# Optimization experiments

Hardware: AMD Instinct MI355X
Metric: run time of the kernel (lower is better)

The kernel has to match this reference:

```python
import jax, jax.numpy as jnp
import numpy as np

# Tsit5 Butcher tableau (Tsitouras 2011), 5th-order solution weights.
C2, C3, C4, C5 = 0.161, 0.327, 0.9, 0.9800255409045097
A21 = 0.161
A31, A32 = -0.008480655492356989, 0.335480655492357
A41, A42, A43 = 2.8971530571054935, -6.359448489975075, 4.3622954328695815
A51, A52, A53, A54 = 5.325864828439257, -11.748883564062828, 7.4955393428898365, -0.09249506636175525
A61, A62, A63, A64, A65 = 5.86145544294642, -12.92096931784711, 8.159367898576159, -0.071584973281401, -0.028269050394068383
B1, B2, B3, B4, B5, B6 = 0.09646076681806523, 0.01, 0.4798896504144996, 1.379008574103742, -3.290069515436081, 2.324710524099774


def setup_inputs() -> dict:
    key = jax.random.key(0)
    k0, k1, k2, k3 = jax.random.split(key, 4)
    B, D, W, T = 2048, 64, 128, 50
    y0 = jax.random.normal(k0, (B, D), dtype=jnp.float32)
    ts = (jnp.arange(T, dtype=jnp.float32)) * 0.02  # t0=0, t1=0.98, dt0=0.02
    # equinox-style MLP params (Linear stores weight as [out, in]); scaled for stability
    w0 = jax.random.normal(k1, (W, D + 1), dtype=jnp.float32) / np.sqrt(D + 1)
    b0 = jnp.zeros((W,), dtype=jnp.float32)
    w1 = jax.random.normal(k2, (W, W), dtype=jnp.float32) / np.sqrt(W)
    b1 = jnp.zeros((W,), dtype=jnp.float32)
    w2 = jax.random.normal(k3, (D, W), dtype=jnp.float32) / np.sqrt(W)
    b2 = jnp.zeros((D,), dtype=jnp.float32)
    return {"y0": y0, "ts": ts, "w0": w0, "b0": b0, "w1": w1, "b1": b1, "w2": w2, "b2": b2}


def reference(y0, ts, w0, b0, w1, b1, w2, b2):
    # dynamics f(t, y) = MLP(concat([t, y])), vectorized over batch
    def dyn(t, y):
        tcol = jnp.full((y.shape[0], 1), t, dtype=y.dtype)
        inp = jnp.concatenate([tcol, y], axis=1)           # [B, D+1]
        h = jax.nn.relu(inp @ w0.T + b0)                    # [B, W]
        h = jax.nn.relu(h @ w1.T + b1)                      # [B, W]
        return h @ w2.T + b2                                # [B, D]

    dt = ts[1] - ts[0]

    def step(y, t):
        k1 = dyn(t, y)
        k2 = dyn(t + C2 * dt, y + dt * (A21 * k1))
        k3 = dyn(t + C3 * dt, y + dt * (A31 * k1 + A32 * k2))
        k4 = dyn(t + C4 * dt, y + dt * (A41 * k1 + A42 * k2 + A43 * k3))
        k5 = dyn(t + C5 * dt, y + dt * (A51 * k1 + A52 * k2 + A53 * k3 + A54 * k4))
        k6 = dyn(t + dt, y + dt * (A61 * k1 + A62 * k2 + A63 * k3 + A64 * k4 + A65 * k5))
        y_new = y + dt * (B1 * k1 + B2 * k2 + B3 * k3 + B4 * k4 + B5 * k5 + B6 * k6)
        return y_new, None

    yT, _ = jax.lax.scan(step, y0, ts[:-1])  # 49 constant-size Tsit5 steps
    return yT
```

## Files before the change

### kernel.cpp

```cpp
#include <hip/hip_runtime.h>

typedef __attribute__((ext_vector_type(8))) short short8;
typedef __attribute__((ext_vector_type(4))) float f32x4;
typedef __attribute__((ext_vector_type(4))) unsigned short ushort4v;

__device__ __constant__ float dA2[6][6] = {
  {0.f, 0.f, 0.f, 0.f, 0.f, 0.f},
  {0.161f, 0.f, 0.f, 0.f, 0.f, 0.f},
  {-0.008480655492356989f, 0.335480655492357f, 0.f, 0.f, 0.f, 0.f},
  {2.8971530571054935f, -6.359448489975075f, 4.3622954328695815f, 0.f, 0.f, 0.f},
  {5.325864828439257f, -11.748883564062828f, 7.4955393428898365f, -0.09249506636175525f, 0.f, 0.f},
  {5.86145544294642f, -12.92096931784711f, 8.159367898576159f, -0.071584973281401f, -0.028269050394068383f, 0.f}
};
__device__ __constant__ float dC6[6] = {0.f, 0.161f, 0.327f, 0.9f, 0.9800255409045097f, 1.0f};
__device__ __constant__ float dB6v[6] = {0.09646076681806523f, 0.01f, 0.4798896504144996f,
                                         1.379008574103742f, -3.290069515436081f, 2.324710524099774f};

#define NSTEPS 49
#define XS 136

__device__ __forceinline__ unsigned short f2bf(float f) {
    unsigned u = __builtin_bit_cast(unsigned, f);
    u += 0x7fff + ((u >> 16) & 1);
    return (unsigned short)(u >> 16);
}

extern "C" __global__ void __launch_bounds__(512, 1)
node_solve(const float* __restrict__ y0, const float* __restrict__ ts,
           const float* __restrict__ gw0, const float* __restrict__ gb0,
           const float* __restrict__ gw1, const float* __restrict__ gb1,
           const float* __restrict__ gw2, const float* __restrict__ gb2,
           float* __restrict__ out)
{
    __shared__ __align__(16) unsigned short sSI[16 * XS];
    __shared__ __align__(16) unsigned short sH1[16 * XS];
    __shared__ __align__(16) unsigned short sH2[16 * XS];

    const int tid  = threadIdx.x;
    const int w    = tid >> 6;
    const int lane = tid & 63;
    const int q    = lane >> 4;
    const int c    = lane & 15;
    const int nt   = 16 * w;
    const int n3   = 16 * w;
    const int row0 = blockIdx.x * 16;

    for (int i = tid; i < 16 * 48; i += 512) {
        int r = i / 48, j = i - r * 48;
        ((int*)sSI)[r * 68 + j] = 0;
    }
    __syncthreads();
    for (int i = tid; i < 16 * 64; i += 512) {
        int r = i >> 6, d = i & 63;
        sSI[r * XS + d] = f2bf(y0[(size_t)(row0 + r) * 64 + d]);
    }
    if (tid < 16) sSI[tid * XS + 64] = f2bf(ts[0]);

    short8 wL1[3], wL2[4], wL3[4];
    float  bL1, bL2, bL3 = 0.f;
    {
        const int n = nt + c;
        #pragma unroll
        for (int ks = 0; ks < 3; ++ks) {
            short8 v;
            #pragma unroll
            for (int j = 0; j < 8; ++j) {
                const int k = ks * 32 + q * 8 + j;
                float f = (k < 64) ? gw0[n * 65 + 1 + k] : (k == 64 ? gw0[n * 65] : 0.f);
                v[j] = (short)f2bf(f);
            }
            wL1[ks] = v;
        }
        #pragma unroll
        for (int ks = 0; ks < 4; ++ks) {
            short8 v;
            #pragma unroll
            for (int j = 0; j < 8; ++j) v[j] = (short)f2bf(gw1[n * 128 + ks * 32 + q * 8 + j]);
            wL2[ks] = v;
        }
        bL1 = gb0[n]; bL2 = gb1[n];
    }
    if (w < 4) {
        const int n = n3 + c;
        #pragma unroll
        for (int ks = 0; ks < 4; ++ks) {
            short8 v;
            #pragma unroll
            for (int j = 0; j < 8; ++j) v[j] = (short)f2bf(gw2[n * 128 + ks * 32 + q * 8 + j]);
            wL3[ks] = v;
        }
        bL3 = gb2[n];
    }

    float sy[4] = {0.f, 0.f, 0.f, 0.f};
    float k0[4], k1[4], k2[4], k3[4], k4[4], k5[4];
    #pragma unroll
    for (int r = 0; r < 4; ++r) { k0[r]=0.f; k1[r]=0.f; k2[r]=0.f; k3[r]=0.f; k4[r]=0.f; k5[r]=0.f; }
    if (w < 4) {
        #pragma unroll
        for (int r = 0; r < 4; ++r)
            sy[r] = y0[(size_t)(row0 + c) * 64 + n3 + q * 4 + r];
    }

    const float ts0 = ts[0];
    const float dtv = ts[1] - ts[0];

    __syncthreads();

    #pragma unroll 1
    for (int step = 0; step < NSTEPS; ++step) {
        const float tstep = ts0 + (float)step * dtv;

        #pragma unroll
        for (int s = 0; s < 6; ++s) {
            {
                const unsigned short* xb = &sSI[c * XS + q * 8];
                short8 x0 = *(const short8*)(xb);
                short8 x1 = *(const short8*)(xb + 32);
                short8 x2 = *(const short8*)(xb + 64);
                f32x4 a0 = {0.f,0.f,0.f,0.f};
                a0 = __builtin_amdgcn_mfma_f32_16x16x32_bf16(wL1[0], x0, a0, 0, 0, 0);
                a0 = __builtin_amdgcn_mfma_f32_16x16x32_bf16(wL1[1], x1, a0, 0, 0, 0);
                a0 = __builtin_amdgcn_mfma_f32_16x16x32_bf16(wL1[2], x2, a0, 0, 0, 0);
                ushort4v o0;
                #pragma unroll
                for (int r = 0; r < 4; ++r) o0[r] = f2bf(fmaxf(a0[r] + bL1, 0.f));
                *(ushort4v*)(&sH1[c * XS + nt + q * 4]) = o0;
            }
            __syncthreads();

            {
                const unsigned short* xb = &sH1[c * XS + q * 8];
                short8 x0 = *(const short8*)(xb);
                short8 x1 = *(const short8*)(xb + 32);
                short8 x2 = *(const short8*)(xb + 64);
                short8 x3 = *(const short8*)(xb + 96);
                f32x4 a0 = {0.f,0.f,0.f,0.f}, a1 = {0.f,0.f,0.f,0.f};
                a0 = __builtin_amdgcn_mfma_f32_16x16x32_bf16(wL2[0], x0, a0, 0, 0, 0);
                a1 = __builtin_amdgcn_mfma_f32_16x16x32_bf16(wL2[1], x1, a1, 0, 0, 0);
                a0 = __builtin_amdgcn_mfma_f32_16x16x32_bf16(wL2[2], x2, a0, 0, 0, 0);
                a1 = __builtin_amdgcn_mfma_f32_16x16x32_bf16(wL2[3], x3, a1, 0, 0, 0);
                a0 = a0 + a1;
                ushort4v o0;
                #pragma unroll
                for (int r = 0; r < 4; ++r) o0[r] = f2bf(fmaxf(a0[r] + bL2, 0.f));
                *(ushort4v*)(&sH2[c * XS + nt + q * 4]) = o0;
            }
            __syncthreads();

            if (w < 4) {
                const unsigned short* xb = &sH2[c * XS + q * 8];
                short8 x0 = *(const short8*)(xb);
                short8 x1 = *(const short8*)(xb + 32);
                short8 x2 = *(const short8*)(xb + 64);
                short8 x3 = *(const short8*)(xb + 96);
                f32x4 aa = {0.f,0.f,0.f,0.f}, ab = {0.f,0.f,0.f,0.f};
                aa = __builtin_amdgcn_mfma_f32_16x16x32_bf16(wL3[0], x0, aa, 0, 0, 0);
                ab = __builtin_amdgcn_mfma_f32_16x16x32_bf16(wL3[1], x1, ab, 0, 0, 0);
                aa = __builtin_amdgcn_mfma_f32_16x16x32_bf16(wL3[2], x2, aa, 0, 0, 0);
                ab = __builtin_amdgcn_mfma_f32_16x16x32_bf16(wL3[3], x3, ab, 0, 0, 0);
                aa = aa + ab;

                float kv[4];
                #pragma unroll
                for (int r = 0; r < 4; ++r) kv[r] = aa[r] + bL3;
                if      (s == 0) { k0[0]=kv[0]; k0[1]=kv[1]; k0[2]=kv[2]; k0[3]=kv[3]; }
                else if (s == 1) { k1[0]=kv[0]; k1[1]=kv[1]; k1[2]=kv[2]; k1[3]=kv[3]; }
                else if (s == 2) { k2[0]=kv[0]; k2[1]=kv[1]; k2[2]=kv[2]; k2[3]=kv[3]; }
                else if (s == 3) { k3[0]=kv[0]; k3[1]=kv[1]; k3[2]=kv[2]; k3[3]=kv[3]; }
                else if (s == 4) { k4[0]=kv[0]; k4[1]=kv[1]; k4[2]=kv[2]; k4[3]=kv[3]; }
                else             { k5[0]=kv[0]; k5[1]=kv[1]; k5[2]=kv[2]; k5[3]=kv[3]; }

                float si[4];
                if (s < 5) {
                    const float a0c = dA2[s + 1][0], a1c = dA2[s + 1][1], a2c = dA2[s + 1][2];
                    const float a3c = dA2[s + 1][3], a4c = dA2[s + 1][4], a5c = dA2[s + 1][5];
                    #pragma unroll
                    for (int r = 0; r < 4; ++r)
                        si[r] = sy[r] + dtv * (a0c*k0[r] + a1c*k1[r] + a2c*k2[r]
                                             + a3c*k3[r] + a4c*k4[r] + a5c*k5[r]);
                } else {
                    #pragma unroll
                    for (int r = 0; r < 4; ++r) {
                        sy[r] += dtv * (dB6v[0]*k0[r] + dB6v[1]*k1[r] + dB6v[2]*k2[r]
                                      + dB6v[3]*k3[r] + dB6v[4]*k4[r] + dB6v[5]*k5[r]);
                        si[r] = sy[r];
                    }
                }
                ushort4v ov;
                #pragma unroll
                for (int r = 0; r < 4; ++r) ov[r] = f2bf(si[r]);
                *(ushort4v*)(&sSI[c * XS + n3 + q * 4]) = ov;
                if (w == 0 && q == 0) {
                    const float tn = (s < 5) ? (tstep + dC6[s + 1] * dtv) : (tstep + dtv);
                    sSI[c * XS + 64] = f2bf(tn);
                }
            }
            __syncthreads();
        }
    }

    if (w < 4) {
        float4 v = make_float4(sy[0], sy[1], sy[2], sy[3]);
        *(float4*)(&out[(size_t)(row0 + c) * 64 + n3 + q * 4]) = v;
    }
}

extern "C" void kernel_launch(void* const* d_in, const int* in_sizes, int n_in,
                              void* d_out, int out_size, void* d_ws, size_t ws_size,
                              hipStream_t stream) {
    const float* y0 = (const float*)d_in[0];
    const float* ts = (const float*)d_in[1];
    const float* w0 = (const float*)d_in[2];
    const float* b0 = (const float*)d_in[3];
    const float* w1 = (const float*)d_in[4];
    const float* b1 = (const float*)d_in[5];
    const float* w2 = (const float*)d_in[6];
    const float* b2 = (const float*)d_in[7];
    float* out = (float*)d_out;

    node_solve<<<dim3(128), dim3(512), 0, stream>>>(y0, ts, w0, b0, w1, b1, w2, b2, out);
}
```

Baseline: 254.0 us.

## Run whole Tsit5 MLP solve in one wavefront with register-resident activations

Each block is cut from 8 wavefronts to a single 64-lane wavefront that keeps all three weight matrices in registers. Layer outputs pass straight from MFMA accumulators into the next layer's B operands through a permuted K ordering, so the shared memory and all __syncthreads barriers go away. The t column and layer-0 bias are folded into one extra K slice, and the Butcher coefficients are premultiplied by dt. The trade-off is much higher register pressure and no parallelism across waves within a CU, so only 128 waves run in total and the MFMA chains are serialized.

```diff
diff --git a/kernel.cpp b/kernel.cpp
--- a/kernel.cpp
+++ b/kernel.cpp
@@ -1,209 +1,219 @@
 #include <hip/hip_runtime.h>
 
-typedef __attribute__((ext_vector_type(8))) short short8;
-typedef __attribute__((ext_vector_type(4))) float f32x4;
-typedef __attribute__((ext_vector_type(4))) unsigned short ushort4v;
-
-__device__ __constant__ float dA2[6][6] = {
-  {0.f, 0.f, 0.f, 0.f, 0.f, 0.f},
-  {0.161f, 0.f, 0.f, 0.f, 0.f, 0.f},
-  {-0.008480655492356989f, 0.335480655492357f, 0.f, 0.f, 0.f, 0.f},
-  {2.8971530571054935f, -6.359448489975075f, 4.3622954328695815f, 0.f, 0.f, 0.f},
-  {5.325864828439257f, -11.748883564062828f, 7.4955393428898365f, -0.09249506636175525f, 0.f, 0.f},
-  {5.86145544294642f, -12.92096931784711f, 8.159367898576159f, -0.071584973281401f, -0.028269050394068383f, 0.f}
-};
-__device__ __constant__ float dC6[6] = {0.f, 0.161f, 0.327f, 0.9f, 0.9800255409045097f, 1.0f};
-__device__ __constant__ float dB6v[6] = {0.09646076681806523f, 0.01f, 0.4798896504144996f,
-                                         1.379008574103742f, -3.290069515436081f, 2.324710524099774f};
+typedef __attribute__((ext_vector_type(8))) short   short8;
+typedef __attribute__((ext_vector_type(8))) __bf16  bf16x8;
+typedef __attribute__((ext_vector_type(4))) float   f32x4;
 
 #define NSTEPS 49
-#define XS 136
-
-__device__ __forceinline__ unsigned short f2bf(float f) {
-    unsigned u = __builtin_bit_cast(unsigned, f);
-    u += 0x7fff + ((u >> 16) & 1);
-    return (unsigned short)(u >> 16);
+
+static __device__ __forceinline__ short8 as_s8(bf16x8 v) {
+    return __builtin_bit_cast(short8, v);
 }
 
-extern "C" __global__ void __launch_bounds__(512, 1)
+#define MFMA(A, B, C) __builtin_amdgcn_mfma_f32_16x16x32_bf16((A), (B), (C), 0, 0, 0)
+
+#define BUILD_XS(SRC)                                                     \
+    {                                                                     \
+        bf16x8 v0_, v1_;                                                  \
+        v0_[0] = (__bf16)(SRC)[0][0]; v0_[1] = (__bf16)(SRC)[0][1];       \
+        v0_[2] = (__bf16)(SRC)[0][2]; v0_[3] = (__bf16)(SRC)[0][3];       \
+        v0_[4] = (__bf16)(SRC)[1][0]; v0_[5] = (__bf16)(SRC)[1][1];       \
+        v0_[6] = (__bf16)(SRC)[1][2]; v0_[7] = (__bf16)(SRC)[1][3];       \
+        v1_[0] = (__bf16)(SRC)[2][0]; v1_[1] = (__bf16)(SRC)[2][1];       \
+        v1_[2] = (__bf16)(SRC)[2][2]; v1_[3] = (__bf16)(SRC)[2][3];       \
+        v1_[4] = (__bf16)(SRC)[3][0]; v1_[5] = (__bf16)(SRC)[3][1];       \
+        v1_[6] = (__bf16)(SRC)[3][2]; v1_[7] = (__bf16)(SRC)[3][3];       \
+        xs0 = as_s8(v0_); xs1 = as_s8(v1_);                               \
+    }
+
+#define BUILD_XT(TV)                                                      \
+    {                                                                     \
+        bf16x8 v_;                                                        \
+        _Pragma("unroll") for (int j_ = 0; j_ < 8; ++j_) v_[j_] = (__bf16)0.f; \
+        if (q == 0) { v_[0] = (__bf16)(TV); v_[1] = (__bf16)1.0f; }       \
+        xt = as_s8(v_);                                                   \
+    }
+
+#define MLP_EVAL(KK)                                                      \
+    {                                                                     \
+        const f32x4 zz_ = {0.f, 0.f, 0.f, 0.f};                           \
+        f32x4 a1_[8];                                                     \
+        _Pragma("unroll")                                                 \
+        for (int t_ = 0; t_ < 8; ++t_) {                                  \
+            f32x4 ac_ = MFMA(wA0[t_][0], xs0, zz_);                       \
+            ac_ = MFMA(wA0[t_][1], xs1, ac_);                             \
+            ac_ = MFMA(wA0[t_][2], xt,  ac_);                             \
+            a1_[t_] = ac_;                                                \
+        }                                                                 \
+        short8 xh_[4];                                                    \
+        _Pragma("unroll")                                                 \
+        for (int ks_ = 0; ks_ < 4; ++ks_) {                               \
+            bf16x8 v_;                                                    \
+            v_[0] = (__bf16)fmaxf(a1_[2*ks_  ][0], 0.f);                  \
+            v_[1] = (__bf16)fmaxf(a1_[2*ks_  ][1], 0.f);                  \
+            v_[2] = (__bf16)fmaxf(a1_[2*ks_  ][2], 0.f);                  \
+            v_[3] = (__bf16)fmaxf(a1_[2*ks_  ][3], 0.f);                  \
+            v_[4] = (__bf16)fmaxf(a1_[2*ks_+1][0], 0.f);                  \
+            v_[5] = (__bf16)fmaxf(a1_[2*ks_+1][1], 0.f);                  \
+            v_[6] = (__bf16)fmaxf(a1_[2*ks_+1][2], 0.f);                  \
+            v_[7] = (__bf16)fmaxf(a1_[2*ks_+1][3], 0.f);                  \
+            xh_[ks_] = as_s8(v_);                                         \
+        }                                                                 \
+        f32x4 a2_[8];                                                     \
+        _Pragma("unroll")                                                 \
+        for (int t_ = 0; t_ < 8; ++t_) {                                  \
+            f32x4 ac_ = MFMA(wA1[t_][0], xh_[0], zz_);                    \
+            ac_ = MFMA(wA1[t_][1], xh_[1], ac_);                          \
+            ac_ = MFMA(wA1[t_][2], xh_[2], ac_);                          \
+            ac_ = MFMA(wA1[t_][3], xh_[3], ac_);                          \
+            a2_[t_] = ac_;                                                \
+        }                                                                 \
+        short8 xg_[4];                                                    \
+        _Pragma("unroll")                                                 \
+        for (int ks_ = 0; ks_ < 4; ++ks_) {                               \
+            bf16x8 v_;                                                    \
+            v_[0] = (__bf16)fmaxf(a2_[2*ks_  ][0] + bL2[2*ks_  ], 0.f);   \
+            v_[1] = (__bf16)fmaxf(a2_[2*ks_  ][1] + bL2[2*ks_  ], 0.f);   \
+            v_[2] = (__bf16)fmaxf(a2_[2*ks_  ][2] + bL2[2*ks_  ], 0.f);   \
+            v_[3] = (__bf16)fmaxf(a2_[2*ks_  ][3] + bL2[2*ks_  ], 0.f);   \
+            v_[4] = (__bf16)fmaxf(a2_[2*ks_+1][0] + bL2[2*ks_+1], 0.f);   \
+            v_[5] = (__bf16)fmaxf(a2_[2*ks_+1][1] + bL2[2*ks_+1], 0.f);   \
+            v_[6] = (__bf16)fmaxf(a2_[2*ks_+1][2] + bL2[2*ks_+1], 0.f);   \
+            v_[7] = (__bf16)fmaxf(a2_[2*ks_+1][3] + bL2[2*ks_+1], 0.f);   \
+            xg_[ks_] = as_s8(v_);                                         \
+        }                                                                 \
+        _Pragma("unroll")                                                 \
+        for (int t_ = 0; t_ < 4; ++t_) {                                  \
+            f32x4 ac_ = MFMA(wA2[t_][0], xg_[0], zz_);                    \
+            ac_ = MFMA(wA2[t_][1], xg_[1], ac_);                          \
+            ac_ = MFMA(wA2[t_][2], xg_[2], ac_);                          \
+            ac_ = MFMA(wA2[t_][3], xg_[3], ac_);                          \
+            KK[t_] = ac_ + bL3[t_];                                       \
+        }                                                                 \
+    }
+
+extern "C" __global__ void __launch_bounds__(64, 1)
 node_solve(const float* __restrict__ y0, const float* __restrict__ ts,
            const float* __restrict__ gw0, const float* __restrict__ gb0,
            const float* __restrict__ gw1, const float* __restrict__ gb1,
            const float* __restrict__ gw2, const float* __restrict__ gb2,
            float* __restrict__ out)
 {
-    __shared__ __align__(16) unsigned short sSI[16 * XS];
-    __shared__ __align__(16) unsigned short sH1[16 * XS];
-    __shared__ __align__(16) unsigned short sH2[16 * XS];
-
-    const int tid  = threadIdx.x;
-    const int w    = tid >> 6;
-    const int lane = tid & 63;
+    const int lane = threadIdx.x & 63;
     const int q    = lane >> 4;
     const int c    = lane & 15;
-    const int nt   = 16 * w;
-    const int n3   = 16 * w;
-    const int row0 = blockIdx.x * 16;
-
-    for (int i = tid; i < 16 * 48; i += 512) {
-        int r = i / 48, j = i - r * 48;
-        ((int*)sSI)[r * 68 + j] = 0;
-    }
-    __syncthreads();
-    for (int i = tid; i < 16 * 64; i += 512) {
-        int r = i >> 6, d = i & 63;
-        sSI[r * XS + d] = f2bf(y0[(size_t)(row0 + r) * 64 + d]);
-    }
-    if (tid < 16) sSI[tid * XS + 64] = f2bf(ts[0]);
-
-    short8 wL1[3], wL2[4], wL3[4];
-    float  bL1, bL2, bL3 = 0.f;
-    {
-        const int n = nt + c;
-        #pragma unroll
-        for (int ks = 0; ks < 3; ++ks) {
-            short8 v;
-            #pragma unroll
-            for (int j = 0; j < 8; ++j) {
-                const int k = ks * 32 + q * 8 + j;
-                float f = (k < 64) ? gw0[n * 65 + 1 + k] : (k == 64 ? gw0[n * 65] : 0.f);
-                v[j] = (short)f2bf(f);
-            }
-            wL1[ks] = v;
-        }
+    const int row0 = blockIdx.x << 4;
+
+    short8 wA0[8][3];
+    short8 wA1[8][4];
+    short8 wA2[4][4];
+    float  bL2[8], bL3[4];
+
+    #pragma unroll
+    for (int t = 0; t < 8; ++t) {
+        const int n = 16 * t + c;
+        const float* w0r = gw0 + n * 65 + 1;
+        #pragma unroll
+        for (int ks = 0; ks < 2; ++ks) {
+            bf16x8 v;
+            #pragma unroll
+            for (int j = 0; j < 8; ++j)
+                v[j] = (__bf16)w0r[32*ks + 16*(j>>2) + 4*q + (j&3)];
+            wA0[t][ks] = as_s8(v);
+        }
+        {
+            bf16x8 v;
+            #pragma unroll
+            for (int j = 0; j < 8; ++j) v[j] = (__bf16)0.f;
+            if (q == 0) { v[0] = (__bf16)gw0[n*65]; v[1] = (__bf16)gb0[n]; }
+            wA0[t][2] = as_s8(v);
+        }
+        const float* w1r = gw1 + n * 128;
         #pragma unroll
         for (int ks = 0; ks < 4; ++ks) {
-            short8 v;
-            #pragma unroll
-            for (int j = 0; j < 8; ++j) v[j] = (short)f2bf(gw1[n * 128 + ks * 32 + q * 8 + j]);
-            wL2[ks] = v;
-        }
-        bL1 = gb0[n]; bL2 = gb1[n];
-    }
-    if (w < 4) {
-        const int n = n3 + c;
+            bf16x8 v;
+            #pragma unroll
+            for (int j = 0; j < 8; ++j)
+                v[j] = (__bf16)w1r[32*ks + 16*(j>>2) + 4*q + (j&3)];
+            wA1[t][ks] = as_s8(v);
+        }
+        bL2[t] = gb1[16*t + c];
+    }
+    #pragma unroll
+    for (int t = 0; t < 4; ++t) {
+        const int n = 16 * t + c;
+        const float* w2r = gw2 + n * 128;
         #pragma unroll
         for (int ks = 0; ks < 4; ++ks) {
-            short8 v;
-            #pragma unroll
-            for (int j = 0; j < 8; ++j) v[j] = (short)f2bf(gw2[n * 128 + ks * 32 + q * 8 + j]);
-            wL3[ks] = v;
-        }
-        bL3 = gb2[n];
-    }
-
-    float sy[4] = {0.f, 0.f, 0.f, 0.f};
-    float k0[4], k1[4], k2[4], k3[4], k4[4], k5[4];
-    #pragma unroll
-    for (int r = 0; r < 4; ++r) { k0[r]=0.f; k1[r]=0.f; k2[r]=0.f; k3[r]=0.f; k4[r]=0.f; k5[r]=0.f; }
-    if (w < 4) {
-        #pragma unroll
-        for (int r = 0; r < 4; ++r)
-            sy[r] = y0[(size_t)(row0 + c) * 64 + n3 + q * 4 + r];
-    }
+            bf16x8 v;
+            #pragma unroll
+            for (int j = 0; j < 8; ++j)
+                v[j] = (__bf16)w2r[32*ks + 16*(j>>2) + 4*q + (j&3)];
+            wA2[t][ks] = as_s8(v);
+        }
+        bL3[t] = gb2[16*t + c];
+    }
+
+    f32x4 y[4];
+    #pragma unroll
+    for (int t = 0; t < 4; ++t)
+        y[t] = *(const f32x4*)(y0 + (size_t)(row0 + c) * 64 + 16*t + 4*q);
 
     const float ts0 = ts[0];
     const float dtv = ts[1] - ts[0];
 
-    __syncthreads();
+    const float d21 = dtv * 0.161f;
+    const float d31 = dtv * -0.008480655492356989f, d32 = dtv * 0.335480655492357f;
+    const float d41 = dtv * 2.8971530571054935f,  d42 = dtv * -6.359448489975075f,  d43 = dtv * 4.3622954328695815f;
+    const float d51 = dtv * 5.325864828439257f,   d52 = dtv * -11.748883564062828f, d53 = dtv * 7.4955393428898365f, d54 = dtv * -0.09249506636175525f;
+    const float d61 = dtv * 5.86145544294642f,    d62 = dtv * -12.92096931784711f,  d63 = dtv * 8.159367898576159f,  d64 = dtv * -0.071584973281401f, d65 = dtv * -0.028269050394068383f;
+    const float e1  = dtv * 0.09646076681806523f, e2  = dtv * 0.01f,                e3  = dtv * 0.4798896504144996f;
+    const float e4  = dtv * 1.379008574103742f,   e5  = dtv * -3.290069515436081f,  e6  = dtv * 2.324710524099774f;
+
+    short8 xs0, xs1, xt;
 
     #pragma unroll 1
     for (int step = 0; step < NSTEPS; ++step) {
-        const float tstep = ts0 + (float)step * dtv;
-
-        #pragma unroll
-        for (int s = 0; s < 6; ++s) {
-            {
-                const unsigned short* xb = &sSI[c * XS + q * 8];
-                short8 x0 = *(const short8*)(xb);
-                short8 x1 = *(const short8*)(xb + 32);
-                short8 x2 = *(const short8*)(xb + 64);
-                f32x4 a0 = {0.f,0.f,0.f,0.f};
-                a0 = __builtin_amdgcn_mfma_f32_16x16x32_bf16(wL1[0], x0, a0, 0, 0, 0);
-                a0 = __builtin_amdgcn_mfma_f32_16x16x32_bf16(wL1[1], x1, a0, 0, 0, 0);
-                a0 = __builtin_amdgcn_mfma_f32_16x16x32_bf16(wL1[2], x2, a0, 0, 0, 0);
-                ushort4v o0;
-                #pragma unroll
-                for (int r = 0; r < 4; ++r) o0[r] = f2bf(fmaxf(a0[r] + bL1, 0.f));
-                *(ushort4v*)(&sH1[c * XS + nt + q * 4]) = o0;
-            }
-            __syncthreads();
-
-            {
-                const unsigned short* xb = &sH1[c * XS + q * 8];
-                short8 x0 = *(const short8*)(xb);
-                short8 x1 = *(const short8*)(xb + 32);
-                short8 x2 = *(const short8*)(xb + 64);
-                short8 x3 = *(const short8*)(xb + 96);
-                f32x4 a0 = {0.f,0.f,0.f,0.f}, a1 = {0.f,0.f,0.f,0.f};
-                a0 = __builtin_amdgcn_mfma_f32_16x16x32_bf16(wL2[0], x0, a0, 0, 0, 0);
-                a1 = __builtin_amdgcn_mfma_f32_16x16x32_bf16(wL2[1], x1, a1, 0, 0, 0);
-                a0 = __builtin_amdgcn_mfma_f32_16x16x32_bf16(wL2[2], x2, a0, 0, 0, 0);
-                a1 = __builtin_amdgcn_mfma_f32_16x16x32_bf16(wL2[3], x3, a1, 0, 0, 0);
-                a0 = a0 + a1;
-                ushort4v o0;
-                #pragma unroll
-                for (int r = 0; r < 4; ++r) o0[r] = f2bf(fmaxf(a0[r] + bL2, 0.f));
-                *(ushort4v*)(&sH2[c * XS + nt + q * 4]) = o0;
-            }
-            __syncthreads();
-
-            if (w < 4) {
-                const unsigned short* xb = &sH2[c * XS + q * 8];
-                short8 x0 = *(const short8*)(xb);
-                short8 x1 = *(const short8*)(xb + 32);
-                short8 x2 = *(const short8*)(xb + 64);
-                short8 x3 = *(const short8*)(xb + 96);
-                f32x4 aa = {0.f,0.f,0.f,0.f}, ab = {0.f,0.f,0.f,0.f};
-                aa = __builtin_amdgcn_mfma_f32_16x16x32_bf16(wL3[0], x0, aa, 0, 0, 0);
-                ab = __builtin_amdgcn_mfma_f32_16x16x32_bf16(wL3[1], x1, ab, 0, 0, 0);
-                aa = __builtin_amdgcn_mfma_f32_16x16x32_bf16(wL3[2], x2, aa, 0, 0, 0);
-                ab = __builtin_amdgcn_mfma_f32_16x16x32_bf16(wL3[3], x3, ab, 0, 0, 0);
-                aa = aa + ab;
-
-                float kv[4];
-                #pragma unroll
-                for (int r = 0; r < 4; ++r) kv[r] = aa[r] + bL3;
-                if      (s == 0) { k0[0]=kv[0]; k0[1]=kv[1]; k0[2]=kv[2]; k0[3]=kv[3]; }
-                else if (s == 1) { k1[0]=kv[0]; k1[1]=kv[1]; k1[2]=kv[2]; k1[3]=kv[3]; }
-                else if (s == 2) { k2[0]=kv[0]; k2[1]=kv[1]; k2[2]=kv[2]; k2[3]=kv[3]; }
-                else if (s == 3) { k3[0]=kv[0]; k3[1]=kv[1]; k3[2]=kv[2]; k3[3]=kv[3]; }
-                else if (s == 4) { k4[0]=kv[0]; k4[1]=kv[1]; k4[2]=kv[2]; k4[3]=kv[3]; }
-                else             { k5[0]=kv[0]; k5[1]=kv[1]; k5[2]=kv[2]; k5[3]=kv[3]; }
-
-                float si[4];
-                if (s < 5) {
-                    const float a0c = dA2[s + 1][0], a1c = dA2[s + 1][1], a2c = dA2[s + 1][2];
-                    const float a3c = dA2[s + 1][3], a4c = dA2[s + 1][4], a5c = dA2[s + 1][5];
-                    #pragma unroll
-                    for (int r = 0; r < 4; ++r)
-                        si[r] = sy[r] + dtv * (a0c*k0[r] + a1c*k1[r] + a2c*k2[r]
-                                             + a3c*k3[r] + a4c*k4[r] + a5c*k5[r]);
-                } else {
-                    #pragma unroll
-                    for (int r = 0; r < 4; ++r) {
-                        sy[r] += dtv * (dB6v[0]*k0[r] + dB6v[1]*k1[r] + dB6v[2]*k2[r]
-                                      + dB6v[3]*k3[r] + dB6v[4]*k4[r] + dB6v[5]*k5[r]);
-                        si[r] = sy[r];
-                    }
-                }
-                ushort4v ov;
-                #pragma unroll
-                for (int r = 0; r < 4; ++r) ov[r] = f2bf(si[r]);
-                *(ushort4v*)(&sSI[c * XS + n3 + q * 4]) = ov;
-                if (w == 0 && q == 0) {
-                    const float tn = (s < 5) ? (tstep + dC6[s + 1] * dtv) : (tstep + dtv);
-                    sSI[c * XS + 64] = f2bf(tn);
-                }
-            }
-            __syncthreads();
-        }
-    }
-
-    if (w < 4) {
-        float4 v = make_float4(sy[0], sy[1], sy[2], sy[3]);
-        *(float4*)(&out[(size_t)(row0 + c) * 64 + n3 + q * 4]) = v;
-    }
+        const float t0s = ts0 + (float)step * dtv;
+        f32x4 k0v[4], k1v[4], k2v[4], k3v[4], k4v[4], k5v[4];
+        f32x4 si[4];
+
+        BUILD_XS(y); BUILD_XT(t0s);
+        MLP_EVAL(k0v);
+
+        #pragma unroll
+        for (int t = 0; t < 4; ++t) si[t] = y[t] + d21 * k0v[t];
+        BUILD_XS(si); BUILD_XT(t0s + 0.161f * dtv);
+        MLP_EVAL(k1v);
+
+        #pragma unroll
+        for (int t = 0; t < 4; ++t) si[t] = y[t] + d31*k0v[t] + d32*k1v[t];
+        BUILD_XS(si); BUILD_XT(t0s + 0.327f * dtv);
+        MLP_EVAL(k2v);
+
+        #pragma unroll
+        for (int t = 0; t < 4; ++t) si[t] = y[t] + d41*k0v[t] + d42*k1v[t] + d43*k2v[t];
+        BUILD_XS(si); BUILD_XT(t0s + 0.9f * dtv);
+        MLP_EVAL(k3v);
+
+        #pragma unroll
+        for (int t = 0; t < 4; ++t) si[t] = y[t] + d51*k0v[t] + d52*k1v[t] + d53*k2v[t] + d54*k3v[t];
+        BUILD_XS(si); BUILD_XT(t0s + 0.9800255409045097f * dtv);
+        MLP_EVAL(k4v);
+
+        #pragma unroll
+        for (int t = 0; t < 4; ++t) si[t] = y[t] + d61*k0v[t] + d62*k1v[t] + d63*k2v[t] + d64*k3v[t] + d65*k4v[t];
+        BUILD_XS(si); BUILD_XT(t0s + dtv);
+        MLP_EVAL(k5v);
+
+        #pragma unroll
+        for (int t = 0; t < 4; ++t)
+            y[t] = y[t] + e1*k0v[t] + e2*k1v[t] + e3*k2v[t] + e4*k3v[t] + e5*k4v[t] + e6*k5v[t];
+    }
+
+    #pragma unroll
+    for (int t = 0; t < 4; ++t)
+        *(f32x4*)(out + (size_t)(row0 + c) * 64 + 16*t + 4*q) = y[t];
 }
 
 extern "C" void kernel_launch(void* const* d_in, const int* in_sizes, int n_in,
@@ -219,5 +229,5 @@
     const float* b2 = (const float*)d_in[7];
     float* out = (float*)d_out;
 
-    node_solve<<<dim3(128), dim3(512), 0, stream>>>(y0, ts, w0, b0, w1, b1, w2, b2, out);
+    node_solve<<<dim3(128), dim3(64), 0, stream>>>(y0, ts, w0, b0, w1, b1, w2, b2, out);
 }
```

After: 474.1 us. 86.6% more time.
